# Kernel optimization log

Measured on AMD Instinct MI355X. Metric: run time of the kernel, lower is better.

## Reference

```python
import jax, jax.numpy as jnp
import numpy as np

DIM = 1024
N_HEADS = 16
HEAD_DIM = DIM // N_HEADS
B, T = 2, 2048


def setup_inputs() -> dict:
    key = jax.random.key(0)
    ks = jax.random.split(key, 5)
    x = jax.random.normal(ks[0], (B, T, DIM), dtype=jnp.float32)
    s = DIM ** -0.5
    Wq = jax.random.normal(ks[1], (DIM, DIM), dtype=jnp.float32) * s
    Wk = jax.random.normal(ks[2], (DIM, DIM), dtype=jnp.float32) * s
    Wv = jax.random.normal(ks[3], (DIM, DIM), dtype=jnp.float32) * s
    Wo = jax.random.normal(ks[4], (DIM, DIM), dtype=jnp.float32) * s
    # causal mask: 1 where attendable, 0 where masked (masked_fill on mask==0)
    mask = jnp.tril(jnp.ones((T, T), dtype=jnp.int32))[None, None, :, :]
    return {"x": x, "Wq": Wq, "Wk": Wk, "Wv": Wv, "Wo": Wo, "mask": mask}


def _rope_tables(seq_len, dim, dtype):
    inv_freq = 1.0 / (10000.0 ** (jnp.arange(0, dim, 2, dtype=jnp.float32) / dim))
    t = jnp.arange(seq_len, dtype=jnp.float32)
    freqs = jnp.outer(t, inv_freq)               # [T, dim/2]
    emb = jnp.concatenate([freqs, freqs], -1)    # [T, dim]
    return jnp.cos(emb).astype(dtype), jnp.sin(emb).astype(dtype)


def _rotate_half(t):
    h = t.shape[-1] // 2
    return jnp.concatenate([-t[..., h:], t[..., :h]], axis=-1)


def reference(x, Wq, Wk, Wv, Wo, mask):
    Bq, Tq, C = x.shape
    H, Dh = N_HEADS, C // N_HEADS
    q = (x @ Wq.T).reshape(Bq, Tq, H, Dh)
    k = (x @ Wk.T).reshape(Bq, Tq, H, Dh)
    v = (x @ Wv.T).reshape(Bq, Tq, H, Dh)
    cos, sin = _rope_tables(Tq, Dh, x.dtype)
    cos = cos[None, :, None, :]   # [1,T,1,Dh]
    sin = sin[None, :, None, :]
    q = q * cos + _rotate_half(q) * sin
    k = k * cos + _rotate_half(k) * sin
    scale = Dh ** -0.5
    # [B,H,T,T]
    attn = jnp.einsum('bqhd,bkhd->bhqk', q, k) * scale
    attn = jnp.where(mask == 0, jnp.float32(-jnp.inf).astype(attn.dtype), attn)
    attn = jax.nn.softmax(attn, axis=-1)
    out = jnp.einsum('bhqk,bkhd->bqhd', attn, v).reshape(Bq, Tq, C)
    return out @ Wo.T
```

## Files before the change

### kernel.cpp

```cpp
#include <hip/hip_runtime.h>
#include <stdint.h>


typedef float  f32x4  __attribute__((ext_vector_type(4)));
typedef __bf16 bf16x8 __attribute__((ext_vector_type(8)));
typedef __bf16 bf16x4 __attribute__((ext_vector_type(4)));

#define GLDS16(gp, lp)                                                         \
  __builtin_amdgcn_global_load_lds(                                            \
      (const __attribute__((address_space(1))) void*)(gp),                     \
      (__attribute__((address_space(3))) void*)(lp), 16, 0, 0)

static __device__ __forceinline__ f32x4 zero4() {
  f32x4 z = {0.f, 0.f, 0.f, 0.f};
  return z;
}

static __device__ __forceinline__ bf16x8 cvt8(const float* __restrict__ p) {
  f32x4 u = *(const f32x4*)p;
  f32x4 v = *(const f32x4*)(p + 4);
  bf16x8 o;
#pragma unroll
  for (int j = 0; j < 4; ++j) o[j] = (__bf16)u[j];
#pragma unroll
  for (int j = 0; j < 4; ++j) o[4 + j] = (__bf16)v[j];
  return o;
}

__global__ __launch_bounds__(256) void prep(
    const float* __restrict__ x,
    const float* __restrict__ Wq, const float* __restrict__ Wk,
    const float* __restrict__ Wv, const float* __restrict__ Wo,
    __bf16* __restrict__ xb, __bf16* __restrict__ Wb)
{
  size_t g = ((size_t)blockIdx.x * 256 + threadIdx.x) * 8;
  if (g < (size_t)4194304) {
    *(bf16x8*)&xb[g] = cvt8(x + g);
  } else {
    size_t j = g - 4194304;
    int w = (int)(j >> 20);
    size_t off = j & 1048575;
    const float* src = (w == 0) ? Wq : (w == 1) ? Wk : (w == 2) ? Wv : Wo;
    *(bf16x8*)&Wb[(size_t)w * 1048576 + off] = cvt8(src + off);
  }
}

__global__ __launch_bounds__(256) void gemm_qkv(
    const __bf16* __restrict__ xb, const __bf16* __restrict__ Wb,
    __bf16* __restrict__ Qp, __bf16* __restrict__ Kp, __bf16* __restrict__ Vt)
{
  __shared__ __bf16 As[128 * 32];
  __shared__ __bf16 Bs[128 * 32];
  __shared__ __bf16 Es[4 * 16 * 72];

  const int tid  = threadIdx.x;
  const int lane = tid & 63;
  const int wid  = tid >> 6;
  const int quad = lane >> 4;
  const int l16  = lane & 15;
  const int wm   = (wid >> 1) * 64;
  const int wn   = (wid & 1) * 64;

  const int lin = blockIdx.x;
  const int n0  = (lin & 7) * 128;
  const int r2  = lin >> 3;
  const int z   = r2 % 3;
  const int m0  = (r2 / 3) * 128;
  const __bf16* Bt = Wb + (size_t)z * 1048576;

  const int r0 = tid >> 2, c0 = tid & 3;
  const int r1 = (tid + 256) >> 2;

  f32x4 acc[4][4];
  for (int i = 0; i < 4; ++i)
    for (int j = 0; j < 4; ++j) acc[i][j] = zero4();

  for (int k0 = 0; k0 < 1024; k0 += 32) {
    __syncthreads();
    GLDS16(xb + (size_t)(m0 + r0) * 1024 + k0 + c0 * 8, &As[(size_t)tid * 8]);
    GLDS16(xb + (size_t)(m0 + r1) * 1024 + k0 + c0 * 8, &As[(size_t)(tid + 256) * 8]);
    GLDS16(Bt + (size_t)(n0 + r0) * 1024 + k0 + c0 * 8, &Bs[(size_t)tid * 8]);
    GLDS16(Bt + (size_t)(n0 + r1) * 1024 + k0 + c0 * 8, &Bs[(size_t)(tid + 256) * 8]);
    __syncthreads();

    bf16x8 af[4], bfr[4];
    for (int i = 0; i < 4; ++i)
      af[i] = *(const bf16x8*)&As[(wm + i * 16 + l16) * 32 + quad * 8];
    for (int i = 0; i < 4; ++i)
      bfr[i] = *(const bf16x8*)&Bs[(wn + i * 16 + l16) * 32 + quad * 8];
    for (int mt = 0; mt < 4; ++mt)
      for (int nt = 0; nt < 4; ++nt)
        acc[mt][nt] = __builtin_amdgcn_mfma_f32_16x16x32_bf16(
            af[mt], bfr[nt], acc[mt][nt], 0, 0, 0);
  }

  const int h = (n0 + wn) >> 6;
  __bf16* es = &Es[wid * 1152];
  const int rl = lane >> 3, ch = lane & 7;

  if (z < 2) {
    const float c0f = -13.287712379549449f / 32.0f;
    const float f0 = exp2f((float)l16 * c0f);
    const float f1 = exp2f((float)(16 + l16) * c0f);
    const float SC = (z == 0) ? 0.125f * 1.44269504088896340736f : 1.0f;
    for (int mt = 0; mt < 4; ++mt)
      for (int r = 0; r < 4; ++r) {
        int gm = m0 + wm + mt * 16 + 4 * quad + r;
        float t = (float)(gm & 2047);
        for (int nt = 0; nt < 2; ++nt) {
          float ang = t * (nt ? f1 : f0);
          float cv = __cosf(ang) * SC, sv = __sinf(ang) * SC;
          float lo = acc[mt][nt][r], hi = acc[mt][nt + 2][r];
          acc[mt][nt][r]     = lo * cv - hi * sv;
          acc[mt][nt + 2][r] = hi * cv + lo * sv;
        }
      }
    __bf16* dst = (z == 0) ? Qp : Kp;
    for (int mt = 0; mt < 4; ++mt) {
      for (int nt = 0; nt < 4; ++nt)
        for (int r = 0; r < 4; ++r)
          es[(4 * quad + r) * 72 + nt * 16 + l16] = (__bf16)acc[mt][nt][r];
      size_t g0 = (size_t)(m0 + wm + mt * 16 + rl) * 1024 + n0 + wn + ch * 8;
      *(bf16x8*)&dst[g0]            = *(const bf16x8*)&es[rl * 72 + ch * 8];
      *(bf16x8*)&dst[g0 + 8 * 1024] = *(const bf16x8*)&es[(rl + 8) * 72 + ch * 8];
    }
  } else {
    const int b = m0 >> 11;
    const size_t hb = (size_t)(b * 16 + h) * 64;
    const int tt = (m0 + wm) & 2047;
    for (int nt = 0; nt < 4; ++nt) {
      for (int mt = 0; mt < 4; ++mt)
        for (int r = 0; r < 4; ++r)
          es[l16 * 72 + mt * 16 + 4 * quad + r] = (__bf16)acc[mt][nt][r];
      size_t g0 = (hb + nt * 16 + rl) * 2048 + tt + ch * 8;
      *(bf16x8*)&Vt[g0]                     = *(const bf16x8*)&es[rl * 72 + ch * 8];
      *(bf16x8*)&Vt[g0 + (size_t)8 * 2048]  = *(const bf16x8*)&es[(rl + 8) * 72 + ch * 8];
    }
  }
}

__global__ __launch_bounds__(256) void attn_fwd(
    __bf16* QA, const __bf16* __restrict__ Kp,
    const __bf16* __restrict__ Vt)
{
  __shared__ __bf16 Ks[64 * 72];
  __shared__ __bf16 Vs[64 * 72];
  __shared__ __bf16 Ps[64 * 72];

  const int tid  = threadIdx.x;
  const int lane = tid & 63, wid = tid >> 6;
  const int quad = lane >> 4, l16 = lane & 15;

  const int L  = blockIdx.x;
  const int Lp = (L & 7) * 64 + (L >> 3);
  const int bh = Lp >> 4;
  const int xq = Lp & 15;
  const int b = bh >> 4, h = bh & 15;

  const size_t rowb = (size_t)b * 2048;
  const __bf16* Vb = Vt + (size_t)bh * 64 * 2048;

  const int sr0 = tid >> 3, sc0 = tid & 7;
  const int sr1 = (tid + 256) >> 3;

  for (int pass = 0; pass < 2; ++pass) {
    const int qb = pass ? (31 - xq) : xq;
    const int q0 = qb * 64;

    bf16x8 qa[2];
    for (int ks = 0; ks < 2; ++ks)
      qa[ks] = *(const bf16x8*)
          &QA[(rowb + q0 + wid * 16 + l16) * 1024 + h * 64 + ks * 32 + quad * 8];

    f32x4 oacc[4];
    for (int i = 0; i < 4; ++i) oacc[i] = zero4();
    float m_i = -1e30f, l_i = 0.f;

    const int kcmax = qb;

    bf16x8 k0v = *(const bf16x8*)&Kp[(rowb + sr0) * 1024 + h * 64 + sc0 * 8];
    bf16x8 k1v = *(const bf16x8*)&Kp[(rowb + sr1) * 1024 + h * 64 + sc0 * 8];
    bf16x8 v0v = *(const bf16x8*)&Vb[(size_t)sr0 * 2048 + sc0 * 8];
    bf16x8 v1v = *(const bf16x8*)&Vb[(size_t)sr1 * 2048 + sc0 * 8];

    for (int kc = 0; kc <= kcmax; ++kc) {
      __syncthreads();
      *(bf16x8*)&Ks[sr0 * 72 + sc0 * 8] = k0v;
      *(bf16x8*)&Ks[sr1 * 72 + sc0 * 8] = k1v;
      *(bf16x8*)&Vs[sr0 * 72 + sc0 * 8] = v0v;
      *(bf16x8*)&Vs[sr1 * 72 + sc0 * 8] = v1v;
      __syncthreads();

      if (kc < kcmax) {
        const int kn = kc + 1;
        k0v = *(const bf16x8*)&Kp[(rowb + kn * 64 + sr0) * 1024 + h * 64 + sc0 * 8];
        k1v = *(const bf16x8*)&Kp[(rowb + kn * 64 + sr1) * 1024 + h * 64 + sc0 * 8];
        v0v = *(const bf16x8*)&Vb[(size_t)sr0 * 2048 + kn * 64 + sc0 * 8];
        v1v = *(const bf16x8*)&Vb[(size_t)sr1 * 2048 + kn * 64 + sc0 * 8];
      }

      f32x4 sacc[4];
      for (int i = 0; i < 4; ++i) sacc[i] = zero4();
      __builtin_amdgcn_s_setprio(1);
      for (int ks = 0; ks < 2; ++ks) {
        bf16x8 qf = qa[ks];
        for (int mt = 0; mt < 4; ++mt) {
          bf16x8 kf = *(const bf16x8*)
              &Ks[(mt * 16 + l16) * 72 + ks * 32 + quad * 8];
          sacc[mt] = __builtin_amdgcn_mfma_f32_16x16x32_bf16(
              kf, qf, sacc[mt], 0, 0, 0);
        }
      }
      __builtin_amdgcn_s_setprio(0);

      const bool diag = (kc == kcmax);
      float rmax = -1e30f;
      const int iq = wid * 16 + l16;
      for (int mt = 0; mt < 4; ++mt)
        for (int r = 0; r < 4; ++r) {
          float s = sacc[mt][r];
          if (diag && (mt * 16 + 4 * quad + r > iq)) s = -1e30f;
          sacc[mt][r] = s;
          rmax = fmaxf(rmax, s);
        }
      rmax = fmaxf(rmax, __shfl_xor(rmax, 16, 64));
      rmax = fmaxf(rmax, __shfl_xor(rmax, 32, 64));

      const bool noresc = __all(rmax <= m_i + 8.0f);
      float alpha = 1.0f;
      if (!noresc) {
        float nm = fmaxf(m_i, rmax);
        alpha = __builtin_amdgcn_exp2f(m_i - nm);
        m_i = nm;
      }

      float rsum = 0.f;
      for (int mt = 0; mt < 4; ++mt) {
        bf16x4 pw;
        for (int r = 0; r < 4; ++r) {
          float p = __builtin_amdgcn_exp2f(sacc[mt][r] - m_i);
          rsum += p;
          pw[r] = (__bf16)p;
        }
        *(bf16x4*)&Ps[iq * 72 + mt * 16 + 4 * quad] = pw;
      }
      rsum += __shfl_xor(rsum, 16, 64);
      rsum += __shfl_xor(rsum, 32, 64);

      if (!noresc) {
        l_i = l_i * alpha + rsum;
        for (int r = 0; r < 4; ++r) {
          float a_r = __shfl(alpha, 4 * quad + r, 64);
          for (int nt = 0; nt < 4; ++nt) oacc[nt][r] *= a_r;
        }
      } else {
        l_i += rsum;
      }

      __builtin_amdgcn_s_setprio(1);
      for (int ks = 0; ks < 2; ++ks) {
        bf16x8 pf = *(const bf16x8*)
            &Ps[(wid * 16 + l16) * 72 + ks * 32 + quad * 8];
        for (int nt = 0; nt < 4; ++nt) {
          bf16x8 vf = *(const bf16x8*)
              &Vs[(nt * 16 + l16) * 72 + ks * 32 + quad * 8];
          oacc[nt] = __builtin_amdgcn_mfma_f32_16x16x32_bf16(
              pf, vf, oacc[nt], 0, 0, 0);
        }
      }
      __builtin_amdgcn_s_setprio(0);
    }

    {
      float invl = 1.0f / l_i;
      for (int r = 0; r < 4; ++r) {
        float inv_r = __shfl(invl, 4 * quad + r, 64);
        for (int nt = 0; nt < 4; ++nt)
          Ps[(wid * 16 + 4 * quad + r) * 72 + nt * 16 + l16] =
              (__bf16)(oacc[nt][r] * inv_r);
      }
    }
    __syncthreads();
    {
      int row = tid >> 3, ch = tid & 7;
      size_t g0 = (rowb + q0 + row) * 1024 + h * 64 + ch * 8;
      *(bf16x8*)&QA[g0]                   = *(const bf16x8*)&Ps[row * 72 + ch * 8];
      *(bf16x8*)&QA[g0 + (size_t)32 * 1024] =
          *(const bf16x8*)&Ps[(row + 32) * 72 + ch * 8];
    }
    __syncthreads();
  }
}

__global__ __launch_bounds__(256) void gemm_out(
    const __bf16* __restrict__ AO, const __bf16* __restrict__ Wob,
    float* __restrict__ Of)
{
  __shared__ __bf16 As[128 * 32];
  __shared__ __bf16 Bs[128 * 32];
  __shared__ float  EsF[4 * 16 * 68];

  const int tid  = threadIdx.x;
  const int lane = tid & 63;
  const int wid  = tid >> 6;
  const int quad = lane >> 4;
  const int l16  = lane & 15;
  const int wm   = (wid >> 1) * 64;
  const int wn   = (wid & 1) * 64;
  const int lin = blockIdx.x;
  const int n0  = (lin & 7) * 128;
  const int m0  = (lin >> 3) * 128;

  const int r0 = tid >> 2, c0 = tid & 3;
  const int r1 = (tid + 256) >> 2;

  f32x4 acc[4][4];
  for (int i = 0; i < 4; ++i)
    for (int j = 0; j < 4; ++j) acc[i][j] = zero4();

  for (int k0 = 0; k0 < 1024; k0 += 32) {
    __syncthreads();
    GLDS16(AO  + (size_t)(m0 + r0) * 1024 + k0 + c0 * 8, &As[(size_t)tid * 8]);
    GLDS16(AO  + (size_t)(m0 + r1) * 1024 + k0 + c0 * 8, &As[(size_t)(tid + 256) * 8]);
    GLDS16(Wob + (size_t)(n0 + r0) * 1024 + k0 + c0 * 8, &Bs[(size_t)tid * 8]);
    GLDS16(Wob + (size_t)(n0 + r1) * 1024 + k0 + c0 * 8, &Bs[(size_t)(tid + 256) * 8]);
    __syncthreads();

    bf16x8 af[4], bfr[4];
    for (int i = 0; i < 4; ++i)
      af[i] = *(const bf16x8*)&As[(wm + i * 16 + l16) * 32 + quad * 8];
    for (int i = 0; i < 4; ++i)
      bfr[i] = *(const bf16x8*)&Bs[(wn + i * 16 + l16) * 32 + quad * 8];
    for (int mt = 0; mt < 4; ++mt)
      for (int nt = 0; nt < 4; ++nt)
        acc[mt][nt] = __builtin_amdgcn_mfma_f32_16x16x32_bf16(
            af[mt], bfr[nt], acc[mt][nt], 0, 0, 0);
  }

  float* es = &EsF[wid * 1088];
  const int rl = lane >> 4, ch = lane & 15;
  for (int mt = 0; mt < 4; ++mt) {
    for (int nt = 0; nt < 4; ++nt)
      for (int r = 0; r < 4; ++r)
        es[(4 * quad + r) * 68 + nt * 16 + l16] = acc[mt][nt][r];
    size_t g0 = (size_t)(m0 + wm + mt * 16 + rl) * 1024 + n0 + wn + ch * 4;
    *(f32x4*)&Of[g0]             = *(const f32x4*)&es[rl * 68 + ch * 4];
    *(f32x4*)&Of[g0 + 4 * 1024]  = *(const f32x4*)&es[(rl + 4) * 68 + ch * 4];
    *(f32x4*)&Of[g0 + 8 * 1024]  = *(const f32x4*)&es[(rl + 8) * 68 + ch * 4];
    *(f32x4*)&Of[g0 + 12 * 1024] = *(const f32x4*)&es[(rl + 12) * 68 + ch * 4];
  }
}

__global__ __launch_bounds__(256) void copy_bf16x8(
    const __bf16* __restrict__ src, __bf16* __restrict__ dst)
{
  size_t i = ((size_t)blockIdx.x * 256 + threadIdx.x) * 8;
  *(bf16x8*)&dst[i] = *(const bf16x8*)&src[i];
}

extern "C" void kernel_launch(void* const* d_in, const int* in_sizes, int n_in,
                              void* d_out, int out_size, void* d_ws, size_t ws_size,
                              hipStream_t stream) {
  const float* x  = (const float*)d_in[0];
  const float* Wq = (const float*)d_in[1];
  const float* Wk = (const float*)d_in[2];
  const float* Wv = (const float*)d_in[3];
  const float* Wo = (const float*)d_in[4];
  float* out = (float*)d_out;

  const size_t NELT = (size_t)4194304;
  __bf16* Qp = (__bf16*)d_ws;
  __bf16* Kp = Qp + NELT;
  __bf16* Vt = Kp + NELT;
  __bf16* xb = (__bf16*)d_out;
  __bf16* Wb = xb + NELT;

  prep<<<dim3(4096), 256, 0, stream>>>(x, Wq, Wk, Wv, Wo, xb, Wb);
  gemm_qkv<<<dim3(768), 256, 0, stream>>>(xb, Wb, Qp, Kp, Vt);
  attn_fwd<<<dim3(512), 256, 0, stream>>>(Qp, Kp, Vt);
  copy_bf16x8<<<dim3(512), 256, 0, stream>>>(Wb + 3 * NELT / 4, Kp);
  gemm_out<<<dim3(256), 256, 0, stream>>>(Qp, Kp, out);
}
```

Baseline: 200.3 us.

## Process both paired query tiles in one KV sweep with double-buffered LDS

The attention kernel no longer runs two sequential passes over the low and high query blocks. It streams K/V tiles once and computes both query tiles against each loaded tile, which roughly halves K/V global loads and LDS staging for the low tile. The K/V tiles are now double-buffered in LDS with a two-ahead register prefetch, so each iteration needs one barrier instead of two. The cost is more registers (two accumulator and Q sets) and more LDS, which may lower occupancy.

```diff
diff --git a/kernel.cpp b/kernel.cpp
--- a/kernel.cpp
+++ b/kernel.cpp
@@ -143,9 +143,10 @@
     __bf16* QA, const __bf16* __restrict__ Kp,
     const __bf16* __restrict__ Vt)
 {
-  __shared__ __bf16 Ks[64 * 72];
-  __shared__ __bf16 Vs[64 * 72];
-  __shared__ __bf16 Ps[64 * 72];
+  __shared__ __bf16 Ks[2][64 * 72];
+  __shared__ __bf16 Vs[2][64 * 72];
+  __shared__ __bf16 PsA[64 * 72];
+  __shared__ __bf16 PsB[64 * 72];
 
   const int tid  = threadIdx.x;
   const int lane = tid & 63, wid = tid >> 6;
@@ -163,132 +164,216 @@
   const int sr0 = tid >> 3, sc0 = tid & 7;
   const int sr1 = (tid + 256) >> 3;
 
-  for (int pass = 0; pass < 2; ++pass) {
-    const int qb = pass ? (31 - xq) : xq;
-    const int q0 = qb * 64;
-
-    bf16x8 qa[2];
-    for (int ks = 0; ks < 2; ++ks)
-      qa[ks] = *(const bf16x8*)
-          &QA[(rowb + q0 + wid * 16 + l16) * 1024 + h * 64 + ks * 32 + quad * 8];
-
-    f32x4 oacc[4];
-    for (int i = 0; i < 4; ++i) oacc[i] = zero4();
-    float m_i = -1e30f, l_i = 0.f;
-
-    const int kcmax = qb;
-
-    bf16x8 k0v = *(const bf16x8*)&Kp[(rowb + sr0) * 1024 + h * 64 + sc0 * 8];
-    bf16x8 k1v = *(const bf16x8*)&Kp[(rowb + sr1) * 1024 + h * 64 + sc0 * 8];
-    bf16x8 v0v = *(const bf16x8*)&Vb[(size_t)sr0 * 2048 + sc0 * 8];
-    bf16x8 v1v = *(const bf16x8*)&Vb[(size_t)sr1 * 2048 + sc0 * 8];
-
-    for (int kc = 0; kc <= kcmax; ++kc) {
-      __syncthreads();
-      *(bf16x8*)&Ks[sr0 * 72 + sc0 * 8] = k0v;
-      *(bf16x8*)&Ks[sr1 * 72 + sc0 * 8] = k1v;
-      *(bf16x8*)&Vs[sr0 * 72 + sc0 * 8] = v0v;
-      *(bf16x8*)&Vs[sr1 * 72 + sc0 * 8] = v1v;
-      __syncthreads();
-
-      if (kc < kcmax) {
-        const int kn = kc + 1;
-        k0v = *(const bf16x8*)&Kp[(rowb + kn * 64 + sr0) * 1024 + h * 64 + sc0 * 8];
-        k1v = *(const bf16x8*)&Kp[(rowb + kn * 64 + sr1) * 1024 + h * 64 + sc0 * 8];
-        v0v = *(const bf16x8*)&Vb[(size_t)sr0 * 2048 + kn * 64 + sc0 * 8];
-        v1v = *(const bf16x8*)&Vb[(size_t)sr1 * 2048 + kn * 64 + sc0 * 8];
-      }
-
-      f32x4 sacc[4];
-      for (int i = 0; i < 4; ++i) sacc[i] = zero4();
-      __builtin_amdgcn_s_setprio(1);
+  const int qlo = xq, qhi = 31 - xq;
+  const int q0lo = qlo * 64, q0hi = qhi * 64;
+  const int iq = wid * 16 + l16;
+
+  bf16x8 qaL[2], qaH[2];
+  for (int ks = 0; ks < 2; ++ks) {
+    qaL[ks] = *(const bf16x8*)
+        &QA[(rowb + q0lo + iq) * 1024 + h * 64 + ks * 32 + quad * 8];
+    qaH[ks] = *(const bf16x8*)
+        &QA[(rowb + q0hi + iq) * 1024 + h * 64 + ks * 32 + quad * 8];
+  }
+
+  f32x4 oaccL[4], oaccH[4];
+  for (int i = 0; i < 4; ++i) { oaccL[i] = zero4(); oaccH[i] = zero4(); }
+  float mL = -1e30f, lL = 0.f, mH = -1e30f, lH = 0.f;
+
+  bf16x8 k0v, k1v, v0v, v1v;
+  k0v = *(const bf16x8*)&Kp[(rowb + sr0) * 1024 + h * 64 + sc0 * 8];
+  k1v = *(const bf16x8*)&Kp[(rowb + sr1) * 1024 + h * 64 + sc0 * 8];
+  v0v = *(const bf16x8*)&Vb[(size_t)sr0 * 2048 + sc0 * 8];
+  v1v = *(const bf16x8*)&Vb[(size_t)sr1 * 2048 + sc0 * 8];
+  *(bf16x8*)&Ks[0][sr0 * 72 + sc0 * 8] = k0v;
+  *(bf16x8*)&Ks[0][sr1 * 72 + sc0 * 8] = k1v;
+  *(bf16x8*)&Vs[0][sr0 * 72 + sc0 * 8] = v0v;
+  *(bf16x8*)&Vs[0][sr1 * 72 + sc0 * 8] = v1v;
+  k0v = *(const bf16x8*)&Kp[(rowb + 64 + sr0) * 1024 + h * 64 + sc0 * 8];
+  k1v = *(const bf16x8*)&Kp[(rowb + 64 + sr1) * 1024 + h * 64 + sc0 * 8];
+  v0v = *(const bf16x8*)&Vb[(size_t)sr0 * 2048 + 64 + sc0 * 8];
+  v1v = *(const bf16x8*)&Vb[(size_t)sr1 * 2048 + 64 + sc0 * 8];
+  __syncthreads();
+
+  for (int kc = 0; kc <= qhi; ++kc) {
+    const int c = kc & 1;
+    if (kc < qhi) {
+      *(bf16x8*)&Ks[c ^ 1][sr0 * 72 + sc0 * 8] = k0v;
+      *(bf16x8*)&Ks[c ^ 1][sr1 * 72 + sc0 * 8] = k1v;
+      *(bf16x8*)&Vs[c ^ 1][sr0 * 72 + sc0 * 8] = v0v;
+      *(bf16x8*)&Vs[c ^ 1][sr1 * 72 + sc0 * 8] = v1v;
+    }
+    if (kc + 2 <= qhi) {
+      const int kn = kc + 2;
+      k0v = *(const bf16x8*)&Kp[(rowb + kn * 64 + sr0) * 1024 + h * 64 + sc0 * 8];
+      k1v = *(const bf16x8*)&Kp[(rowb + kn * 64 + sr1) * 1024 + h * 64 + sc0 * 8];
+      v0v = *(const bf16x8*)&Vb[(size_t)sr0 * 2048 + kn * 64 + sc0 * 8];
+      v1v = *(const bf16x8*)&Vb[(size_t)sr1 * 2048 + kn * 64 + sc0 * 8];
+    }
+
+    const bool doLo = (kc <= qlo);
+
+    f32x4 saccH[4], saccL[4];
+    for (int i = 0; i < 4; ++i) saccH[i] = zero4();
+    __builtin_amdgcn_s_setprio(1);
+    for (int ks = 0; ks < 2; ++ks) {
+      bf16x8 qf = qaH[ks];
+      for (int mt = 0; mt < 4; ++mt) {
+        bf16x8 kf = *(const bf16x8*)
+            &Ks[c][(mt * 16 + l16) * 72 + ks * 32 + quad * 8];
+        saccH[mt] = __builtin_amdgcn_mfma_f32_16x16x32_bf16(
+            kf, qf, saccH[mt], 0, 0, 0);
+      }
+    }
+    if (doLo) {
+      for (int i = 0; i < 4; ++i) saccL[i] = zero4();
       for (int ks = 0; ks < 2; ++ks) {
-        bf16x8 qf = qa[ks];
+        bf16x8 qf = qaL[ks];
         for (int mt = 0; mt < 4; ++mt) {
           bf16x8 kf = *(const bf16x8*)
-              &Ks[(mt * 16 + l16) * 72 + ks * 32 + quad * 8];
-          sacc[mt] = __builtin_amdgcn_mfma_f32_16x16x32_bf16(
-              kf, qf, sacc[mt], 0, 0, 0);
-        }
-      }
-      __builtin_amdgcn_s_setprio(0);
-
-      const bool diag = (kc == kcmax);
+              &Ks[c][(mt * 16 + l16) * 72 + ks * 32 + quad * 8];
+          saccL[mt] = __builtin_amdgcn_mfma_f32_16x16x32_bf16(
+              kf, qf, saccL[mt], 0, 0, 0);
+        }
+      }
+    }
+    __builtin_amdgcn_s_setprio(0);
+
+    {
+      const bool diag = (kc == qhi);
       float rmax = -1e30f;
-      const int iq = wid * 16 + l16;
       for (int mt = 0; mt < 4; ++mt)
         for (int r = 0; r < 4; ++r) {
-          float s = sacc[mt][r];
+          float s = saccH[mt][r];
           if (diag && (mt * 16 + 4 * quad + r > iq)) s = -1e30f;
-          sacc[mt][r] = s;
+          saccH[mt][r] = s;
           rmax = fmaxf(rmax, s);
         }
       rmax = fmaxf(rmax, __shfl_xor(rmax, 16, 64));
       rmax = fmaxf(rmax, __shfl_xor(rmax, 32, 64));
-
-      const bool noresc = __all(rmax <= m_i + 8.0f);
+      const bool noresc = __all(rmax <= mH + 8.0f);
       float alpha = 1.0f;
       if (!noresc) {
-        float nm = fmaxf(m_i, rmax);
-        alpha = __builtin_amdgcn_exp2f(m_i - nm);
-        m_i = nm;
-      }
-
+        float nm = fmaxf(mH, rmax);
+        alpha = __builtin_amdgcn_exp2f(mH - nm);
+        mH = nm;
+      }
       float rsum = 0.f;
       for (int mt = 0; mt < 4; ++mt) {
         bf16x4 pw;
         for (int r = 0; r < 4; ++r) {
-          float p = __builtin_amdgcn_exp2f(sacc[mt][r] - m_i);
+          float p = __builtin_amdgcn_exp2f(saccH[mt][r] - mH);
           rsum += p;
           pw[r] = (__bf16)p;
         }
-        *(bf16x4*)&Ps[iq * 72 + mt * 16 + 4 * quad] = pw;
+        *(bf16x4*)&PsB[iq * 72 + mt * 16 + 4 * quad] = pw;
       }
       rsum += __shfl_xor(rsum, 16, 64);
       rsum += __shfl_xor(rsum, 32, 64);
-
       if (!noresc) {
-        l_i = l_i * alpha + rsum;
+        lH = lH * alpha + rsum;
         for (int r = 0; r < 4; ++r) {
           float a_r = __shfl(alpha, 4 * quad + r, 64);
-          for (int nt = 0; nt < 4; ++nt) oacc[nt][r] *= a_r;
+          for (int nt = 0; nt < 4; ++nt) oaccH[nt][r] *= a_r;
         }
       } else {
-        l_i += rsum;
-      }
-
-      __builtin_amdgcn_s_setprio(1);
+        lH += rsum;
+      }
+    }
+    if (doLo) {
+      const bool diag = (kc == qlo);
+      float rmax = -1e30f;
+      for (int mt = 0; mt < 4; ++mt)
+        for (int r = 0; r < 4; ++r) {
+          float s = saccL[mt][r];
+          if (diag && (mt * 16 + 4 * quad + r > iq)) s = -1e30f;
+          saccL[mt][r] = s;
+          rmax = fmaxf(rmax, s);
+        }
+      rmax = fmaxf(rmax, __shfl_xor(rmax, 16, 64));
+      rmax = fmaxf(rmax, __shfl_xor(rmax, 32, 64));
+      const bool noresc = __all(rmax <= mL + 8.0f);
+      float alpha = 1.0f;
+      if (!noresc) {
+        float nm = fmaxf(mL, rmax);
+        alpha = __builtin_amdgcn_exp2f(mL - nm);
+        mL = nm;
+      }
+      float rsum = 0.f;
+      for (int mt = 0; mt < 4; ++mt) {
+        bf16x4 pw;
+        for (int r = 0; r < 4; ++r) {
+          float p = __builtin_amdgcn_exp2f(saccL[mt][r] - mL);
+          rsum += p;
+          pw[r] = (__bf16)p;
+        }
+        *(bf16x4*)&PsA[iq * 72 + mt * 16 + 4 * quad] = pw;
+      }
+      rsum += __shfl_xor(rsum, 16, 64);
+      rsum += __shfl_xor(rsum, 32, 64);
+      if (!noresc) {
+        lL = lL * alpha + rsum;
+        for (int r = 0; r < 4; ++r) {
+          float a_r = __shfl(alpha, 4 * quad + r, 64);
+          for (int nt = 0; nt < 4; ++nt) oaccL[nt][r] *= a_r;
+        }
+      } else {
+        lL += rsum;
+      }
+    }
+
+    __builtin_amdgcn_s_setprio(1);
+    for (int ks = 0; ks < 2; ++ks) {
+      bf16x8 pf = *(const bf16x8*)
+          &PsB[(wid * 16 + l16) * 72 + ks * 32 + quad * 8];
+      for (int nt = 0; nt < 4; ++nt) {
+        bf16x8 vf = *(const bf16x8*)
+            &Vs[c][(nt * 16 + l16) * 72 + ks * 32 + quad * 8];
+        oaccH[nt] = __builtin_amdgcn_mfma_f32_16x16x32_bf16(
+            pf, vf, oaccH[nt], 0, 0, 0);
+      }
+    }
+    if (doLo) {
       for (int ks = 0; ks < 2; ++ks) {
         bf16x8 pf = *(const bf16x8*)
-            &Ps[(wid * 16 + l16) * 72 + ks * 32 + quad * 8];
+            &PsA[(wid * 16 + l16) * 72 + ks * 32 + quad * 8];
         for (int nt = 0; nt < 4; ++nt) {
           bf16x8 vf = *(const bf16x8*)
-              &Vs[(nt * 16 + l16) * 72 + ks * 32 + quad * 8];
-          oacc[nt] = __builtin_amdgcn_mfma_f32_16x16x32_bf16(
-              pf, vf, oacc[nt], 0, 0, 0);
-        }
-      }
-      __builtin_amdgcn_s_setprio(0);
-    }
-
-    {
-      float invl = 1.0f / l_i;
-      for (int r = 0; r < 4; ++r) {
-        float inv_r = __shfl(invl, 4 * quad + r, 64);
-        for (int nt = 0; nt < 4; ++nt)
-          Ps[(wid * 16 + 4 * quad + r) * 72 + nt * 16 + l16] =
-              (__bf16)(oacc[nt][r] * inv_r);
-      }
-    }
+              &Vs[c][(nt * 16 + l16) * 72 + ks * 32 + quad * 8];
+          oaccL[nt] = __builtin_amdgcn_mfma_f32_16x16x32_bf16(
+              pf, vf, oaccL[nt], 0, 0, 0);
+        }
+      }
+    }
+    __builtin_amdgcn_s_setprio(0);
+
     __syncthreads();
-    {
-      int row = tid >> 3, ch = tid & 7;
-      size_t g0 = (rowb + q0 + row) * 1024 + h * 64 + ch * 8;
-      *(bf16x8*)&QA[g0]                   = *(const bf16x8*)&Ps[row * 72 + ch * 8];
-      *(bf16x8*)&QA[g0 + (size_t)32 * 1024] =
-          *(const bf16x8*)&Ps[(row + 32) * 72 + ch * 8];
-    }
-    __syncthreads();
+  }
+
+  {
+    float invL = 1.0f / lL, invH = 1.0f / lH;
+    for (int r = 0; r < 4; ++r) {
+      float iLr = __shfl(invL, 4 * quad + r, 64);
+      float iHr = __shfl(invH, 4 * quad + r, 64);
+      for (int nt = 0; nt < 4; ++nt) {
+        PsA[(wid * 16 + 4 * quad + r) * 72 + nt * 16 + l16] =
+            (__bf16)(oaccL[nt][r] * iLr);
+        PsB[(wid * 16 + 4 * quad + r) * 72 + nt * 16 + l16] =
+            (__bf16)(oaccH[nt][r] * iHr);
+      }
+    }
+  }
+  __syncthreads();
+  {
+    int row = tid >> 3, ch = tid & 7;
+    size_t gLo = (rowb + q0lo + row) * 1024 + h * 64 + ch * 8;
+    size_t gHi = (rowb + q0hi + row) * 1024 + h * 64 + ch * 8;
+    *(bf16x8*)&QA[gLo] = *(const bf16x8*)&PsA[row * 72 + ch * 8];
+    *(bf16x8*)&QA[gLo + (size_t)32 * 1024] =
+        *(const bf16x8*)&PsA[(row + 32) * 72 + ch * 8];
+    *(bf16x8*)&QA[gHi] = *(const bf16x8*)&PsB[row * 72 + ch * 8];
+    *(bf16x8*)&QA[gHi + (size_t)32 * 1024] =
+        *(const bf16x8*)&PsB[(row + 32) * 72 + ch * 8];
   }
 }
 
```

Measured after the change: 198.4 us. About the same (-0.9%).
